# Performance work log

Measured on AMD Instinct MI355X. Metric: run time of the kernel, lower is better.

## Reference

```python
import jax, jax.numpy as jnp
import numpy as np

N, B, K, LATENT, HIDDEN, OUT = 100000, 256, 32, 64, 256, 32


def setup_inputs() -> dict:
    key = jax.random.key(0)
    ks = jax.random.split(key, 7)
    z = jax.random.normal(ks[0], (B, K, LATENT), dtype=jnp.float32)
    s = jax.random.uniform(ks[1], (N, K), dtype=jnp.float32)
    batch = jax.random.randint(ks[2], (N,), 0, B, dtype=jnp.int64)
    W1 = jax.random.normal(ks[3], (LATENT, HIDDEN), dtype=jnp.float32) / np.sqrt(LATENT)
    b1 = jnp.zeros((HIDDEN,), dtype=jnp.float32)
    W2 = jax.random.normal(ks[4], (HIDDEN, OUT), dtype=jnp.float32) / np.sqrt(HIDDEN)
    b2 = jnp.zeros((OUT,), dtype=jnp.float32)
    return {"z": z, "s": s, "batch": batch, "W1": W1, "b1": b1, "W2": W2, "b2": b2}


def reference(z, s, batch, W1, b1, W2, b2):
    # z: [B, K, L] per-graph cluster latents; batch: [N] node->graph; s: [N, K]
    z_gather = z[batch]                                  # [N, K, L]
    node_lat = jnp.einsum("nk,nkl->nl", s, z_gather)     # [N, L]
    h = jax.nn.relu(node_lat @ W1 + b1)                  # [N, HIDDEN]
    return h @ W2 + b2                                   # [N, OUT]
```

## Files before the change

kernel.cpp:

```cpp
#include <hip/hip_runtime.h>
#include <hip/hip_fp16.h>


using f16   = _Float16;
using f16x4 = __attribute__((ext_vector_type(4))) _Float16;
using f16x8 = __attribute__((ext_vector_type(8))) _Float16;
using f32x4 = __attribute__((ext_vector_type(4))) float;

constexpr int NN     = 100000;
constexpr int KK     = 32;
constexpr int LATENT = 64;
constexpr int HIDDEN = 256;
constexpr int OUTD   = 32;

constexpr int BLOCK    = 256;
constexpr int W2F_OFF  = 16384;
constexpr int NPREP    = 25;
constexpr int SEGCAP   = 64;


__global__ __launch_bounds__(1024)
void prep(const float* __restrict__ W1,
          const float* __restrict__ W2,
          const int*   __restrict__ batch,
          f16* __restrict__ wsf,
          int* __restrict__ hist,
          int* __restrict__ perm2) {
    __shared__ int lcnt[256];
    const int t = threadIdx.x;
    if (t < 256) lcnt[t] = 0;

    const int gid = blockIdx.x * 1024 + t;
    if (gid < 16384) {
        const int j = gid & 7, lane = (gid >> 3) & 63, g = gid >> 9;
        const int ks = g & 1, nt = g >> 1;
        const int k = ks * 32 + (lane >> 4) * 8 + j;
        const int c = nt * 16 + (lane & 15);
        wsf[gid] = (f16)W1[k * HIDDEN + c];
    } else if (gid < 16384 + 8192) {
        const int g2 = gid - 16384;
        const int j = g2 & 7, lane = (g2 >> 3) & 63, g = g2 >> 9;
        const int ks = g & 7, nt2 = g >> 3;
        const int k = ks * 32 + (lane >> 4) * 8 + j;
        const int c = nt2 * 16 + (lane & 15);
        wsf[W2F_OFF + g2] = (f16)W2[k * OUTD + c];
    }
    __syncthreads();

    const int n0 = gid * 4;
    int bb[4], slot[4];
    const bool act = n0 < NN;
    if (act) {
        const int4 bv = *(const int4*)(batch + n0);
        bb[0] = bv.x; bb[1] = bv.y; bb[2] = bv.z; bb[3] = bv.w;
        #pragma unroll
        for (int i = 0; i < 4; ++i) slot[i] = atomicAdd(&lcnt[bb[i]], 1);
    }
    if (act) {
        #pragma unroll
        for (int i = 0; i < 4; ++i)
            if (slot[i] < SEGCAP)
                perm2[(bb[i] * NPREP + blockIdx.x) * SEGCAP + slot[i]] = n0 + i;
    }
    __syncthreads();
    if (t < 256) hist[blockIdx.x * 256 + t] = lcnt[t];
}

__global__ __launch_bounds__(BLOCK, 7)
void gnn_decoder(const float* __restrict__ z,
                 const float* __restrict__ s,
                 const f16*   __restrict__ wsf,
                 const int*   __restrict__ hist,
                 const int*   __restrict__ perm2,
                 const float* __restrict__ b1,
                 const float* __restrict__ b2,
                 float*       __restrict__ out)
{
    __shared__ f16 zf[4][64][8];
    __shared__ f16 latlds[4][64][20];
    __shared__ f16 hcf[4][2][64][8];
    __shared__ int sstart[26];

    const int bg    = blockIdx.x >> 3;
    const int chunk = blockIdx.x & 7;

    const int t    = threadIdx.x;
    const int w    = t >> 6;
    const int lane = t & 63;
    const int lrow = lane & 15;
    const int quad = lane >> 4;

    {
        const float* zb = z + (size_t)bg * (KK * LATENT) + quad * 8 * LATENT
                        + w * 16 + lrow;
        f16x8 v;
        #pragma unroll
        for (int j = 0; j < 8; ++j) v[j] = (f16)zb[j * LATENT];
        *(f16x8*)&zf[w][lane][0] = v;
    }

    if (t < 64) {
        const int c = (lane < NPREP) ? hist[lane * 256 + bg] : 0;
        int x = c;
        #pragma unroll
        for (int o = 1; o < 32; o <<= 1) {
            const int y = __shfl_up(x, o);
            if (lane >= o) x += y;
        }
        if (lane < NPREP) sstart[lane] = x - c;
        if (lane == NPREP - 1) sstart[NPREP] = x;
    }
    __syncthreads();

    const int total = sstart[NPREP];
    const int cnt_c = total - chunk * 64;
    if (cnt_c <= 0) return;
    const int cn = cnt_c < 64 ? cnt_c : 64;

    int gs = chunk * 64 + w * 16 + lrow;
    if (gs >= total) gs = total - 1;
    int seg = 0;
    #pragma unroll
    for (int i = 1; i < NPREP; ++i) seg = (gs >= sstart[i]) ? i : seg;
    const int pn = perm2[(bg * NPREP + seg) * SEGCAP + (gs - sstart[seg])];

    f16x8 sA;
    {
        const float4* sp = (const float4*)(s + (size_t)pn * KK + quad * 8);
        const float4 s0 = sp[0], s1 = sp[1];
        sA[0] = (f16)s0.x; sA[1] = (f16)s0.y; sA[2] = (f16)s0.z; sA[3] = (f16)s0.w;
        sA[4] = (f16)s1.x; sA[5] = (f16)s1.y; sA[6] = (f16)s1.z; sA[7] = (f16)s1.w;
    }

    #pragma unroll
    for (int lt = 0; lt < 4; ++lt) {
        const f16x8 zB = *(const f16x8*)&zf[lt][lane][0];
        f32x4 D = (f32x4){0.f, 0.f, 0.f, 0.f};
        D = __builtin_amdgcn_mfma_f32_16x16x32_f16(sA, zB, D, 0, 0, 0);
        f16x4 dv;
        #pragma unroll
        for (int r = 0; r < 4; ++r) dv[r] = (f16)D[r];
        *(f16x4*)&latlds[w][lt * 16 + lrow][quad * 4] = dv;
    }
    __builtin_amdgcn_wave_barrier();

    f16x8 latB0, latB1;
    #pragma unroll
    for (int j = 0; j < 8; ++j) {
        latB0[j] = latlds[w][quad * 8 + j][lrow];
        latB1[j] = latlds[w][32 + quad * 8 + j][lrow];
    }

    const f16x8*  W1f = (const f16x8*)wsf;
    const f16x8*  W2f = (const f16x8*)(wsf + W2F_OFF);
    const float4* b1v = (const float4*)b1;

    f32x4 O0 = (f32x4){0.f, 0.f, 0.f, 0.f};
    f32x4 O1 = (f32x4){0.f, 0.f, 0.f, 0.f};

    #pragma unroll
    for (int ksH = 0; ksH < 8; ++ksH) {
        #pragma unroll
        for (int p = 0; p < 2; ++p) {
            const int ntA = ksH * 2 + p;
            f32x4 C = (f32x4){0.f, 0.f, 0.f, 0.f};
            C = __builtin_amdgcn_mfma_f32_16x16x32_f16(
                    W1f[(ntA * 2 + 0) * 64 + lane], latB0, C, 0, 0, 0);
            C = __builtin_amdgcn_mfma_f32_16x16x32_f16(
                    W1f[(ntA * 2 + 1) * 64 + lane], latB1, C, 0, 0, 0);
            const float4 bq = b1v[ntA * 4 + quad];
            f16x4 hv;
            hv[0] = (f16)fmaxf(C[0] + bq.x, 0.f);
            hv[1] = (f16)fmaxf(C[1] + bq.y, 0.f);
            hv[2] = (f16)fmaxf(C[2] + bq.z, 0.f);
            hv[3] = (f16)fmaxf(C[3] + bq.w, 0.f);
            *(f16x4*)&hcf[w][ksH & 1][(p * 2 + (quad >> 1)) * 16 + lrow][(quad & 1) * 4] = hv;
        }
        __builtin_amdgcn_wave_barrier();
        const f16x8 Ah = *(const f16x8*)&hcf[w][ksH & 1][lane][0];
        O0 = __builtin_amdgcn_mfma_f32_16x16x32_f16(Ah, W2f[(0 * 8 + ksH) * 64 + lane], O0, 0, 0, 0);
        O1 = __builtin_amdgcn_mfma_f32_16x16x32_f16(Ah, W2f[(1 * 8 + ksH) * 64 + lane], O1, 0, 0, 0);
    }

    {
        const float b2a = b2[lrow];
        const float b2b = b2[16 + lrow];
        #pragma unroll
        for (int r = 0; r < 4; ++r) {
            const int m = w * 16 + quad * 4 + r;
            const int pr = __shfl(pn, quad * 4 + r);
            if (m < cn) {
                float* dst = out + (size_t)pr * OUTD;
                dst[lrow]      = O0[r] + b2a;
                dst[16 + lrow] = O1[r] + b2b;
            }
        }
    }
}

extern "C" void kernel_launch(void* const* d_in, const int* in_sizes, int n_in,
                              void* d_out, int out_size, void* d_ws, size_t ws_size,
                              hipStream_t stream) {
    const float* z     = (const float*)d_in[0];
    const float* s     = (const float*)d_in[1];
    const int*   batch = (const int*)d_in[2];
    const float* W1    = (const float*)d_in[3];
    const float* b1    = (const float*)d_in[4];
    const float* W2    = (const float*)d_in[5];
    const float* b2    = (const float*)d_in[6];
    float* out = (float*)d_out;

    f16* wsf   = (f16*)d_ws;
    int* hist  = (int*)((char*)d_ws + 49152);
    int* perm2 = hist + NPREP * 256;

    prep<<<NPREP, 1024, 0, stream>>>(W1, W2, batch, wsf, hist, perm2);
    gnn_decoder<<<256 * 8, BLOCK, 0, stream>>>(z, s, wsf, hist, perm2, b1, b2, out);
}
```

Measured before the change: 103.9 us.

## Transpose histogram layout, do per-wave scan in registers, vectorize latent LDS reads

The per-graph histogram is stored transposed so each block reads its 25 counts contiguously. Every wave now computes the prefix scan redundantly and looks up segment starts with shuffles, which removes the shared sstart array and the block barrier placed before the node gather. The z staging and its barrier move after the s load so they overlap with that latency. The latent tile in LDS is transposed so the B operands are read as single 16-byte vector loads instead of sixteen scalar reads, at the cost of scalar strided writes.

After: 103.0 us. No clear change (-0.8%).

```diff
diff --git a/kernel.cpp b/kernel.cpp
--- a/kernel.cpp
+++ b/kernel.cpp
@@ -24,7 +24,7 @@
           const float* __restrict__ W2,
           const int*   __restrict__ batch,
           f16* __restrict__ wsf,
-          int* __restrict__ hist,
+          int* __restrict__ hist2,
           int* __restrict__ perm2) {
     __shared__ int lcnt[256];
     const int t = threadIdx.x;
@@ -63,23 +63,22 @@
                 perm2[(bb[i] * NPREP + blockIdx.x) * SEGCAP + slot[i]] = n0 + i;
     }
     __syncthreads();
-    if (t < 256) hist[blockIdx.x * 256 + t] = lcnt[t];
+    if (t < 256) hist2[t * 32 + blockIdx.x] = lcnt[t];
 }
 
 __global__ __launch_bounds__(BLOCK, 7)
 void gnn_decoder(const float* __restrict__ z,
                  const float* __restrict__ s,
                  const f16*   __restrict__ wsf,
-                 const int*   __restrict__ hist,
+                 const int*   __restrict__ hist2,
                  const int*   __restrict__ perm2,
                  const float* __restrict__ b1,
                  const float* __restrict__ b2,
                  float*       __restrict__ out)
 {
     __shared__ f16 zf[4][64][8];
-    __shared__ f16 latlds[4][64][20];
+    __shared__ f16 latlds[4][16][72];
     __shared__ f16 hcf[4][2][64][8];
-    __shared__ int sstart[26];
 
     const int bg    = blockIdx.x >> 3;
     const int chunk = blockIdx.x & 7;
@@ -90,39 +89,29 @@
     const int lrow = lane & 15;
     const int quad = lane >> 4;
 
-    {
-        const float* zb = z + (size_t)bg * (KK * LATENT) + quad * 8 * LATENT
-                        + w * 16 + lrow;
-        f16x8 v;
-        #pragma unroll
-        for (int j = 0; j < 8; ++j) v[j] = (f16)zb[j * LATENT];
-        *(f16x8*)&zf[w][lane][0] = v;
-    }
-
-    if (t < 64) {
-        const int c = (lane < NPREP) ? hist[lane * 256 + bg] : 0;
-        int x = c;
-        #pragma unroll
-        for (int o = 1; o < 32; o <<= 1) {
-            const int y = __shfl_up(x, o);
-            if (lane >= o) x += y;
-        }
-        if (lane < NPREP) sstart[lane] = x - c;
-        if (lane == NPREP - 1) sstart[NPREP] = x;
-    }
-    __syncthreads();
-
-    const int total = sstart[NPREP];
+    const int c = (lane < NPREP) ? hist2[bg * 32 + lane] : 0;
+    int x = c;
+    #pragma unroll
+    for (int o = 1; o < 32; o <<= 1) {
+        const int y = __shfl_up(x, o);
+        if (lane >= o) x += y;
+    }
+    const int excl  = x - c;
+    const int total = __shfl(x, NPREP - 1);
+
     const int cnt_c = total - chunk * 64;
     if (cnt_c <= 0) return;
     const int cn = cnt_c < 64 ? cnt_c : 64;
 
     int gs = chunk * 64 + w * 16 + lrow;
     if (gs >= total) gs = total - 1;
-    int seg = 0;
-    #pragma unroll
-    for (int i = 1; i < NPREP; ++i) seg = (gs >= sstart[i]) ? i : seg;
-    const int pn = perm2[(bg * NPREP + seg) * SEGCAP + (gs - sstart[seg])];
+    int seg = 0, base = 0;
+    #pragma unroll
+    for (int i = 1; i < NPREP; ++i) {
+        const int si = __shfl(excl, i);
+        if (gs >= si) { seg = i; base = si; }
+    }
+    const int pn = perm2[(bg * NPREP + seg) * SEGCAP + (gs - base)];
 
     f16x8 sA;
     {
@@ -132,24 +121,30 @@
         sA[4] = (f16)s1.x; sA[5] = (f16)s1.y; sA[6] = (f16)s1.z; sA[7] = (f16)s1.w;
     }
 
+    {
+        const float* zb = z + (size_t)bg * (KK * LATENT) + quad * 8 * LATENT
+                        + w * 16 + lrow;
+        f16x8 v;
+        #pragma unroll
+        for (int j = 0; j < 8; ++j) v[j] = (f16)zb[j * LATENT];
+        *(f16x8*)&zf[w][lane][0] = v;
+    }
+    __syncthreads();
+
     #pragma unroll
     for (int lt = 0; lt < 4; ++lt) {
         const f16x8 zB = *(const f16x8*)&zf[lt][lane][0];
         f32x4 D = (f32x4){0.f, 0.f, 0.f, 0.f};
         D = __builtin_amdgcn_mfma_f32_16x16x32_f16(sA, zB, D, 0, 0, 0);
-        f16x4 dv;
-        #pragma unroll
-        for (int r = 0; r < 4; ++r) dv[r] = (f16)D[r];
-        *(f16x4*)&latlds[w][lt * 16 + lrow][quad * 4] = dv;
+        const int l = lt * 16 + lrow;
+        #pragma unroll
+        for (int r = 0; r < 4; ++r)
+            latlds[w][quad * 4 + r][l] = (f16)D[r];
     }
     __builtin_amdgcn_wave_barrier();
 
-    f16x8 latB0, latB1;
-    #pragma unroll
-    for (int j = 0; j < 8; ++j) {
-        latB0[j] = latlds[w][quad * 8 + j][lrow];
-        latB1[j] = latlds[w][32 + quad * 8 + j][lrow];
-    }
+    const f16x8 latB0 = *(const f16x8*)&latlds[w][lrow][quad * 8];
+    const f16x8 latB1 = *(const f16x8*)&latlds[w][lrow][32 + quad * 8];
 
     const f16x8*  W1f = (const f16x8*)wsf;
     const f16x8*  W2f = (const f16x8*)(wsf + W2F_OFF);
@@ -211,9 +206,9 @@
     float* out = (float*)d_out;
 
     f16* wsf   = (f16*)d_ws;
-    int* hist  = (int*)((char*)d_ws + 49152);
-    int* perm2 = hist + NPREP * 256;
-
-    prep<<<NPREP, 1024, 0, stream>>>(W1, W2, batch, wsf, hist, perm2);
-    gnn_decoder<<<256 * 8, BLOCK, 0, stream>>>(z, s, wsf, hist, perm2, b1, b2, out);
+    int* hist2 = (int*)((char*)d_ws + 49152);
+    int* perm2 = hist2 + 256 * 32;
+
+    prep<<<NPREP, 1024, 0, stream>>>(W1, W2, batch, wsf, hist2, perm2);
+    gnn_decoder<<<256 * 8, BLOCK, 0, stream>>>(z, s, wsf, hist2, perm2, b1, b2, out);
 }
```
